# Optimization experiments

Hardware: AMD Instinct MI355X
Metric: run time of the kernel (lower is better)

## Reference

```python
import jax, jax.numpy as jnp
import numpy as np

# Dimensions (see shape_source)
U, B, D, H = 1024, 8, 512, 8
CHUNK = 32
NC = U // CHUNK          # 32 chunks
R, S, M = 32, 32, 32     # right-context rows, summary, memory
K = 31                   # depthwise conv kernel
Q = R + U + S            # 1088
KV = M + R + U           # 1088
NEG_INF = -1.0e8


def _build_attention_mask():
    """Chunk-wise Emformer mask: True = disallowed connection.
    Q layout: [R right-context rows | U utterance rows | S summary rows].
    KV layout: [M memory cols | R right-context cols | U utterance cols].
    Chunk c attends: memory banks < c, its own right-context col,
    its own chunk plus 1 left-context chunk of utterance."""
    mask = np.ones((Q, KV), dtype=bool)
    for c in range(NC):
        cols = np.zeros(KV, dtype=bool)
        cols[:min(c, M)] = True                    # memory of prior chunks
        cols[M + c] = True                         # this chunk's right context
        lo = max(0, c - 1) * CHUNK                 # 1 chunk of left context
        hi = (c + 1) * CHUNK
        cols[M + R + lo:M + R + hi] = True
        rows = [c] + list(range(R + c * CHUNK, R + (c + 1) * CHUNK)) + [R + U + c]
        mask[np.ix_(rows, np.nonzero(cols)[0])] = False
    return mask


def setup_inputs() -> dict:
    key = jax.random.key(0)
    ks = jax.random.split(key, 16)
    s = D ** -0.5
    inp = {
        'utterance': jax.random.normal(ks[0], (U, B, D), jnp.float32),
        'right_context': jax.random.normal(ks[1], (R, B, D), jnp.float32),
        'summary': jax.random.normal(ks[2], (S, B, D), jnp.float32),
        'memory': jax.random.normal(ks[3], (M, B, D), jnp.float32),
        'w_q': jax.random.normal(ks[4], (D, D), jnp.float32) * s,
        'b_q': jnp.zeros((D,), jnp.float32),
        'w_kv': jax.random.normal(ks[5], (2 * D, D), jnp.float32) * s,
        'b_kv': jnp.zeros((2 * D,), jnp.float32),
        'w_out': jax.random.normal(ks[6], (D, D), jnp.float32) * s,
        'b_out': jnp.zeros((D,), jnp.float32),
        'w_pw1': jax.random.normal(ks[7], (2 * D, D), jnp.float32) * s,
        'b_pw1': jnp.zeros((2 * D,), jnp.float32),
        'w_dw': jax.random.normal(ks[8], (D, 1, K), jnp.float32) * (K ** -0.5),
        'b_dw': jnp.zeros((D,), jnp.float32),
        'ln_g': jnp.ones((D,), jnp.float32),
        'ln_b': jnp.zeros((D,), jnp.float32),
        'w_pw2': jax.random.normal(ks[9], (D, D), jnp.float32) * s,
        'b_pw2': jnp.zeros((D,), jnp.float32),
        'lengths': jax.random.randint(ks[10], (B,), U // 2, U + 1, jnp.int32),
        'attention_mask': jnp.asarray(_build_attention_mask()),
    }
    return inp


def _conv_module(x, w_pw1, b_pw1, w_dw, b_dw, ln_g, ln_b, w_pw2, b_pw2):
    # x: (T, B, C) -> (B, C, T)
    x = x.transpose(1, 2, 0)
    x = jnp.einsum('bct,oc->bot', x, w_pw1) + b_pw1[:, None]
    a, g = jnp.split(x, 2, axis=1)
    x = a * jax.nn.sigmoid(g)                       # GLU over channel dim
    pad = (K - 1) // 2
    x = jax.lax.conv_general_dilated(
        x, w_dw, (1,), [(pad, pad)],
        dimension_numbers=('NCH', 'OIH', 'NCH'),
        feature_group_count=x.shape[1]) + b_dw[:, None]
    x = x.transpose(0, 2, 1)                        # (B, T, C) for LayerNorm
    mu = x.mean(-1, keepdims=True)
    var = ((x - mu) ** 2).mean(-1, keepdims=True)
    x = (x - mu) * jax.lax.rsqrt(var + 1e-5) * ln_g + ln_b
    x = x.transpose(0, 2, 1)
    x = x * jax.nn.sigmoid(x)                       # Swish
    x = jnp.einsum('bct,oc->bot', x, w_pw2) + b_pw2[:, None]
    return x.transpose(2, 0, 1)                     # (T, B, C)


def _emformer_forward(utterance, right_context, summary, memory,
                      w_q, b_q, w_kv, b_kv, w_out, b_out,
                      w_pw1, b_pw1, w_dw, b_dw, ln_g, ln_b, w_pw2, b_pw2,
                      lengths, attention_mask):
    d = D // H
    scaling = d ** -0.5
    q_in = jnp.concatenate([right_context, utterance, summary], axis=0)   # (Q,B,D)
    query = q_in @ w_q.T + b_q
    kv_in = jnp.concatenate([memory, right_context, utterance], axis=0)   # (KV,B,D)
    kv = kv_in @ w_kv.T + b_kv
    key_t, value_t = jnp.split(kv, 2, axis=2)

    def heads(t):  # (T,B,D) -> (B*H, T, d)
        return t.reshape(t.shape[0], B * H, d).transpose(1, 0, 2)

    qh, kh, vh = heads(query) * scaling, heads(key_t), heads(value_t)
    w = jnp.einsum('bqd,bkd->bqk', qh, kh)                                # (B*H,Q,KV)
    w = jnp.where(attention_mask[None], NEG_INF, w)
    # padding mask: pad positions are kv index >= KV - U + length
    pad = jnp.arange(KV)[None, :] >= (KV - U + lengths)[:, None]          # (B,KV)
    w = jnp.where(pad[:, None, :].repeat(H, axis=1).reshape(B * H, 1, KV), NEG_INF, w)
    p = jax.nn.softmax(w, axis=-1)
    attn = jnp.einsum('bqk,bkd->bqd', p, vh)                              # (B*H,Q,d)
    attn = attn.transpose(1, 0, 2).reshape(Q, B, D)
    outputs = attn @ w_out.T + b_out
    out_ru = outputs[:R + U]                                              # (R+U,B,D)
    # conformer convolution module with residual
    conv_out = _conv_module(out_ru, w_pw1, b_pw1, w_dw, b_dw,
                            ln_g, ln_b, w_pw2, b_pw2)
    return out_ru + conv_out


def reference(utterance, right_context, summary, memory,
              w_q, b_q, w_kv, b_kv, w_out, b_out,
              w_pw1, b_pw1, w_dw, b_dw, ln_g, ln_b, w_pw2, b_pw2,
              lengths, attention_mask):
    return _emformer_forward(utterance, right_context, summary, memory,
                             w_q, b_q, w_kv, b_kv, w_out, b_out,
                             w_pw1, b_pw1, w_dw, b_dw, ln_g, ln_b,
                             w_pw2, b_pw2, lengths, attention_mask)
```

## Files before the change

### kernel.cpp

```cpp
#include <hip/hip_runtime.h>
#include <hip/hip_bf16.h>
#include <math.h>

#define TQ    1056
#define TKV   1088

typedef __attribute__((ext_vector_type(8))) short short8;
typedef __attribute__((ext_vector_type(4))) short short4v;
typedef __attribute__((ext_vector_type(4))) float float4v;
typedef unsigned short ushort_t;

__device__ inline ushort_t f2bf(float x){
  union{float f; unsigned u;} v; v.f = x;
  unsigned r = v.u + 0x7fff + ((v.u >> 16) & 1);
  return (ushort_t)(r >> 16);
}
__device__ inline float bf2f(ushort_t h){
  union{unsigned u; float f;} v; v.u = ((unsigned)h) << 16;
  return v.f;
}

__device__ inline void gl_lds16(const ushort_t* g, ushort_t* l){
  __builtin_amdgcn_global_load_lds(
      (const __attribute__((address_space(1))) unsigned int*)g,
      (__attribute__((address_space(3))) unsigned int*)l, 16, 0, 0);
}

struct Cvt9 {
  const float* s[8];
  ushort_t*    d[8];
  const float* wdw;
  float*       wdwT;
  int bstart[9];
};

__global__ __launch_bounds__(256)
void cvt_f32_bf16(Cvt9 a)
{
  int blk = blockIdx.x;
  if (blk >= a.bstart[8]){
    int k = blk - a.bstart[8];
    int c = threadIdx.x;
    a.wdwT[k * 512 + c]       = a.wdw[c * 31 + k];
    a.wdwT[k * 512 + c + 256] = a.wdw[(c + 256) * 31 + k];
    return;
  }
  int seg = 0;
  while (blk >= a.bstart[seg + 1]) ++seg;
  int local = blk - a.bstart[seg];
  int idx = (local * 256 + threadIdx.x) * 4;
  float4v v = *(const float4v*)(a.s[seg] + idx);
  short4v o;
  #pragma unroll
  for (int j = 0; j < 4; ++j) ((ushort_t*)&o)[j] = f2bf(v[j]);
  *(short4v*)(a.d[seg] + idx) = o;
}

template<int MODE, int NX, int NT>
__global__ __launch_bounds__(256)
void gemm_bf16(const ushort_t* __restrict__ A, const ushort_t* __restrict__ Wb,
               const float* __restrict__ bias, const float* __restrict__ bias2,
               const ushort_t* __restrict__ residb,
               float* __restrict__ C0, ushort_t* __restrict__ U0,
               ushort_t* __restrict__ U1, int ny)
{
  constexpr int JN = NT / 32;
  const int blk = blockIdx.x;
  const int xcd = blk & 7;
  const int j   = blk >> 3;
  const int n_idx = j % NX;
  const int m_idx = (j / NX) * 8 + xcd;
  if (m_idx >= ny) return;

  __shared__ __align__(16) ushort_t As[128 * 64];
  __shared__ __align__(16) ushort_t Bs[NT * 64];
  const int tid  = threadIdx.x;
  const int w    = tid >> 6;
  const int lane = tid & 63;
  const int quad = lane >> 4;
  const int l16  = lane & 15;
  const int n0 = n_idx * NT;
  const int m0 = m_idx * 128;
  const int wm = (w >> 1) * 64;
  const int wn = (w & 1) * (NT / 2);
  const int srow = tid >> 3;
  const int skseg = tid & 7;

  float4v acc[4][JN];
  #pragma unroll
  for (int i = 0; i < 4; ++i)
    #pragma unroll
    for (int jj = 0; jj < JN; ++jj)
      acc[i][jj] = (float4v)(0.f);

  for (int kt = 0; kt < 8; ++kt){
    const int k0 = kt * 64;
    #pragma unroll
    for (int s = 0; s < 4; ++s){
      int row = s*32 + srow;
      gl_lds16(A + (size_t)(m0 + row) * 512 + k0 + ((skseg ^ (row & 7)) << 3),
               &As[row * 64 + (skseg << 3)]);
    }
    #pragma unroll
    for (int s = 0; s < NT/32; ++s){
      int row = s*32 + srow;
      gl_lds16(Wb + (size_t)(n0 + row) * 512 + k0 + ((skseg ^ (row & 7)) << 3),
               &Bs[row * 64 + (skseg << 3)]);
    }
    __syncthreads();
    #pragma unroll
    for (int kc = 0; kc < 2; ++kc){
      const int col = (((quad + (kc << 2)) ^ (l16 & 7)) << 3);
      short8 af[4], bf[JN];
      #pragma unroll
      for (int i = 0; i < 4; ++i)
        af[i] = *(const short8*)&As[(wm + i*16 + l16) * 64 + col];
      #pragma unroll
      for (int jj = 0; jj < JN; ++jj)
        bf[jj] = *(const short8*)&Bs[(wn + jj*16 + l16) * 64 + col];
      #pragma unroll
      for (int i = 0; i < 4; ++i)
        #pragma unroll
        for (int jj = 0; jj < JN; ++jj)
          acc[i][jj] = __builtin_amdgcn_mfma_f32_16x16x32_bf16(
                          af[i], bf[jj], acc[i][jj], 0, 0, 0);
    }
    __syncthreads();
  }

  #pragma unroll
  for (int jj = 0; jj < JN; ++jj){
    const int n = n0 + wn + jj*16 + l16;
    const float bn = (MODE == 4) ? (n < 512 ? bias[n] : bias2[n - 512])
                                 : bias[n];
    #pragma unroll
    for (int i = 0; i < 4; ++i){
      #pragma unroll
      for (int reg = 0; reg < 4; ++reg){
        const int m = m0 + wm + i*16 + quad*4 + reg;
        float v = acc[i][jj][reg] + bn;
        if (MODE == 4){
          if (n < 512){
            if (m >= 256){
              int mq = m - 256;
              int t = mq >> 3, b = mq & 7;
              int h = n >> 6, dh = n & 63;
              U0[(((size_t)(b*8 + h)) * TQ + t) * 64 + dh] = f2bf(v * 0.125f);
            }
          } else if (n < 1024){
            int n2 = n - 512;
            int t = m >> 3, b = m & 7;
            int h = n2 >> 6, dh = n2 & 63;
            U1[(((size_t)(b*8 + h)) * TKV + t) * 64 + dh] = f2bf(v);
          } else {
            int n2 = n - 1024;
            int t = m >> 3, b = m & 7;
            int h = n2 >> 6, dh = n2 & 63;
            ((ushort_t*)residb)[(((size_t)(b*8 + h)) * 64 + dh) * TKV + t] = f2bf(v);
          }
        } else if (MODE == 0){
          U0[(size_t)m * 512 + n] = f2bf(v);
        } else {
          v += bf2f(residb[(size_t)m * 512 + n]);
          C0[(size_t)m * 512 + n] = v;
        }
      }
    }
  }
}

__global__ __launch_bounds__(256)
void gemm_pw1_glu(const ushort_t* __restrict__ A, const ushort_t* __restrict__ Wb,
                  const float* __restrict__ bias, ushort_t* __restrict__ G, int ny)
{
  const int blk = blockIdx.x;
  const int xcd = blk & 7;
  const int j   = blk >> 3;
  const int n_idx = j % 8;
  const int m_idx = (j / 8) * 8 + xcd;
  if (m_idx >= ny) return;

  __shared__ __align__(16) ushort_t As [128 * 64];
  __shared__ __align__(16) ushort_t Bsa[64 * 64];
  __shared__ __align__(16) ushort_t Bsg[64 * 64];
  const int tid  = threadIdx.x;
  const int w    = tid >> 6;
  const int lane = tid & 63;
  const int quad = lane >> 4;
  const int l16  = lane & 15;
  const int n0 = n_idx * 64;
  const int m0 = m_idx * 128;
  const int wm = (w >> 1) * 64;
  const int wn = (w & 1) * 32;
  const int srow = tid >> 3;
  const int skseg = tid & 7;

  float4v acca[4][2], accg[4][2];
  #pragma unroll
  for (int i = 0; i < 4; ++i)
    #pragma unroll
    for (int jj = 0; jj < 2; ++jj){
      acca[i][jj] = (float4v)(0.f);
      accg[i][jj] = (float4v)(0.f);
    }

  for (int kt = 0; kt < 8; ++kt){
    const int k0 = kt * 64;
    #pragma unroll
    for (int s = 0; s < 4; ++s){
      int row = s*32 + srow;
      gl_lds16(A + (size_t)(m0 + row) * 512 + k0 + ((skseg ^ (row & 7)) << 3),
               &As[row * 64 + (skseg << 3)]);
    }
    #pragma unroll
    for (int s = 0; s < 2; ++s){
      int row = s*32 + srow;
      gl_lds16(Wb + (size_t)(n0 + row) * 512 + k0 + ((skseg ^ (row & 7)) << 3),
               &Bsa[row * 64 + (skseg << 3)]);
      gl_lds16(Wb + (size_t)(n0 + 512 + row) * 512 + k0 + ((skseg ^ (row & 7)) << 3),
               &Bsg[row * 64 + (skseg << 3)]);
    }
    __syncthreads();
    #pragma unroll
    for (int kc = 0; kc < 2; ++kc){
      const int col = (((quad + (kc << 2)) ^ (l16 & 7)) << 3);
      short8 af[4], ba[2], bg[2];
      #pragma unroll
      for (int i = 0; i < 4; ++i)
        af[i] = *(const short8*)&As[(wm + i*16 + l16) * 64 + col];
      #pragma unroll
      for (int jj = 0; jj < 2; ++jj){
        ba[jj] = *(const short8*)&Bsa[(wn + jj*16 + l16) * 64 + col];
        bg[jj] = *(const short8*)&Bsg[(wn + jj*16 + l16) * 64 + col];
      }
      #pragma unroll
      for (int i = 0; i < 4; ++i)
        #pragma unroll
        for (int jj = 0; jj < 2; ++jj){
          acca[i][jj] = __builtin_amdgcn_mfma_f32_16x16x32_bf16(
                           af[i], ba[jj], acca[i][jj], 0, 0, 0);
          accg[i][jj] = __builtin_amdgcn_mfma_f32_16x16x32_bf16(
                           af[i], bg[jj], accg[i][jj], 0, 0, 0);
        }
    }
    __syncthreads();
  }

  #pragma unroll
  for (int jj = 0; jj < 2; ++jj){
    const int n = n0 + wn + jj*16 + l16;
    const float bna = bias[n];
    const float bng = bias[n + 512];
    #pragma unroll
    for (int i = 0; i < 4; ++i){
      #pragma unroll
      for (int reg = 0; reg < 4; ++reg){
        const int m = m0 + wm + i*16 + quad*4 + reg;
        float a = acca[i][jj][reg] + bna;
        float g = accg[i][jj][reg] + bng;
        G[(size_t)m * 512 + n] = f2bf(a * (1.f / (1.f + __expf(-g))));
      }
    }
  }
}

#define NPAD 72
#define VPAD 136

__global__ __launch_bounds__(256)
void attn_mfma(const ushort_t* __restrict__ qh, const ushort_t* __restrict__ kh,
               const ushort_t* __restrict__ vt, const int* __restrict__ lengths,
               ushort_t* __restrict__ attn_out)
{
  const int bh = blockIdx.x;
  const int c  = blockIdx.y;
  const int b  = bh >> 3, h = bh & 7;
  const int tid = threadIdx.x;
  const int w   = tid >> 6;
  const int lane = tid & 63;
  const int quad = lane >> 4;
  const int l16  = lane & 15;
  const int len  = lengths[b];

  __shared__ __align__(16) ushort_t Qs[48 * NPAD];
  __shared__ __align__(16) ushort_t KP[128 * NPAD];
  __shared__ __align__(16) ushort_t Vt[64 * VPAD];

  const int tb2 = 64 + (c > 0 ? c - 1 : 0) * 32;
  const int tb3 = 64 + c * 32;

  for (int e = tid; e < 384; e += 256){
    int row = e >> 3, sg = (e & 7) * 8;
    short8 v = {0,0,0,0,0,0,0,0};
    if (row == 0)
      v = *(const short8*)&qh[(((size_t)bh) * TQ + c) * 64 + sg];
    else if (row >= 16)
      v = *(const short8*)&qh[(((size_t)bh) * TQ + 32 + c*32 + (row-16)) * 64 + sg];
    *(short8*)&Qs[row * NPAD + sg] = v;
  }
  for (int e = tid; e < 1024; e += 256){
    int row = e >> 3, sg = (e & 7) * 8;
    int slot = row >> 5, jj = row & 31;
    int t = (slot == 0) ? jj : (slot == 1) ? 32 + jj : (slot == 2) ? tb2 + jj : tb3 + jj;
    *(short8*)&KP[row * NPAD + sg] =
        *(const short8*)&kh[(((size_t)bh) * TKV + t) * 64 + sg];
  }
  for (int e = tid; e < 1024; e += 256){
    int dh = e >> 4, sc = (e & 15) * 8;
    int slot = sc >> 5, jj = sc & 31;
    int t = (slot == 0) ? jj : (slot == 1) ? 32 + jj : (slot == 2) ? tb2 + jj : tb3 + jj;
    *(short8*)&Vt[dh * VPAD + sc] =
        *(const short8*)&vt[(((size_t)bh) * 64 + dh) * TKV + t];
  }
  __syncthreads();

  float4v Sf[3][2];
  #pragma unroll
  for (int mt = 0; mt < 3; ++mt)
    #pragma unroll
    for (int jt = 0; jt < 2; ++jt)
      Sf[mt][jt] = (float4v)(0.f);
  #pragma unroll
  for (int kc = 0; kc < 2; ++kc){
    short8 bfr[2];
    #pragma unroll
    for (int jt = 0; jt < 2; ++jt)
      bfr[jt] = *(const short8*)&KP[(w*32 + jt*16 + l16) * NPAD + kc*32 + quad*8];
    #pragma unroll
    for (int mt = 0; mt < 3; ++mt){
      short8 afr = *(const short8*)&Qs[(mt*16 + l16) * NPAD + kc*32 + quad*8];
      #pragma unroll
      for (int jt = 0; jt < 2; ++jt)
        Sf[mt][jt] = __builtin_amdgcn_mfma_f32_16x16x32_bf16(afr, bfr[jt], Sf[mt][jt], 0,0,0);
    }
  }

  bool live[2];
  #pragma unroll
  for (int jt = 0; jt < 2; ++jt){
    int jcol = jt*16 + l16;
    if      (w == 0) live[jt] = (jcol < c);
    else if (w == 1) live[jt] = (jcol == c);
    else if (w == 2) live[jt] = (c > 0) && ((c-1)*32 + jcol < len);
    else             live[jt] = (c*32 + jcol < len);
  }
  ushort_t pb[3][2][4];
  #pragma unroll
  for (int mt = 0; mt < 3; ++mt)
    #pragma unroll
    for (int jt = 0; jt < 2; ++jt)
      #pragma unroll
      for (int r = 0; r < 4; ++r)
        pb[mt][jt][r] = live[jt] ? f2bf(__expf(Sf[mt][jt][r])) : (ushort_t)0;

  __syncthreads();

  #pragma unroll
  for (int mt = 0; mt < 3; ++mt)
    #pragma unroll
    for (int r = 0; r < 4; ++r){
      int row = mt*16 + quad*4 + r;
      KP[row * VPAD + w*32 + l16]      = pb[mt][0][r];
      KP[row * VPAD + w*32 + 16 + l16] = pb[mt][1][r];
    }
  __syncthreads();

  const short8 ones = {0x3F80,0x3F80,0x3F80,0x3F80,0x3F80,0x3F80,0x3F80,0x3F80};
  float4v Of[3], Ls[3];
  #pragma unroll
  for (int mt = 0; mt < 3; ++mt){ Of[mt] = (float4v)(0.f); Ls[mt] = (float4v)(0.f); }
  #pragma unroll
  for (int kc = 0; kc < 4; ++kc){
    short8 bv = *(const short8*)&Vt[(w*16 + l16) * VPAD + kc*32 + quad*8];
    #pragma unroll
    for (int mt = 0; mt < 3; ++mt){
      short8 ap = *(const short8*)&KP[(mt*16 + l16) * VPAD + kc*32 + quad*8];
      Of[mt] = __builtin_amdgcn_mfma_f32_16x16x32_bf16(ap, bv,   Of[mt], 0,0,0);
      Ls[mt] = __builtin_amdgcn_mfma_f32_16x16x32_bf16(ap, ones, Ls[mt], 0,0,0);
    }
  }

  #pragma unroll
  for (int mt = 0; mt < 3; ++mt){
    #pragma unroll
    for (int r = 0; r < 4; ++r){
      int row = mt*16 + quad*4 + r;
      if (mt == 0 && row != 0) continue;
      float o = Of[mt][r] / Ls[mt][r];
      int t = (mt == 0) ? c : 32 + c*32 + (row - 16);
      attn_out[(((size_t)t) * 8 + b) * 512 + h*64 + w*16 + l16] = f2bf(o);
    }
  }
}

__global__ __launch_bounds__(512)
void conv_ln_silu3(const ushort_t* __restrict__ glub,
                   const float* __restrict__ w_dwT, const float* __restrict__ b_dw,
                   const float* __restrict__ ln_g, const float* __restrict__ ln_b,
                   ushort_t* __restrict__ zb)
{
  const int b  = blockIdx.y;
  const int t0 = blockIdx.x * 16;
  const int tid = threadIdx.x;
  __shared__ __align__(16) char smem[47104];
  ushort_t* in_t = (ushort_t*)smem;
  float*    S    = (float*)smem;

  for (int e = tid; e < 2944; e += 512){
    int row = e >> 6, sg = (e & 63) * 8;
    int tt = t0 - 15 + row;
    short8 v = {0,0,0,0,0,0,0,0};
    if (tt >= 0 && tt < TQ)
      v = *(const short8*)&glub[((size_t)tt * 8 + b) * 512 + sg];
    *(short8*)&in_t[row * 512 + sg] = v;
  }
  float wreg[31];
  #pragma unroll
  for (int k = 0; k < 31; ++k) wreg[k] = w_dwT[k * 512 + tid];
  const float bd = b_dw[tid];
  __syncthreads();

  float col[46];
  #pragma unroll 2
  for (int rr = 0; rr < 46; ++rr) col[rr] = bf2f(in_t[rr * 512 + tid]);

  float r[16];
  #pragma unroll
  for (int t = 0; t < 16; ++t){
    float acc = bd;
    #pragma unroll
    for (int k = 0; k < 31; ++k) acc += col[t + k] * wreg[k];
    r[t] = acc;
  }
  __syncthreads();
  #pragma unroll
  for (int t = 0; t < 16; ++t) S[t * 512 + tid] = r[t];
  __syncthreads();

  const int tg = tid >> 5;
  const int l  = tid & 31;
  float s = 0.f;
  #pragma unroll
  for (int i = 0; i < 16; ++i) s += S[tg * 512 + l + 32*i];
  #pragma unroll
  for (int off = 16; off >= 1; off >>= 1) s += __shfl_xor(s, off);
  const float mu = s * (1.f / 512.f);
  float s2 = 0.f;
  #pragma unroll
  for (int i = 0; i < 16; ++i){
    float d = S[tg * 512 + l + 32*i] - mu;
    s2 += d * d;
  }
  #pragma unroll
  for (int off = 16; off >= 1; off >>= 1) s2 += __shfl_xor(s2, off);
  const float rs = rsqrtf(s2 * (1.f / 512.f) + 1e-5f);

  const int c0 = l * 16;
  ushort_t ov[16];
  #pragma unroll
  for (int e = 0; e < 4; ++e){
    float4v xv = *(const float4v*)&S[tg * 512 + c0 + e*4];
    float4v gv = *(const float4v*)&ln_g[c0 + e*4];
    float4v bv = *(const float4v*)&ln_b[c0 + e*4];
    #pragma unroll
    for (int jj = 0; jj < 4; ++jj){
      float xn = (xv[jj] - mu) * rs * gv[jj] + bv[jj];
      ov[e*4 + jj] = f2bf(xn * (1.f / (1.f + __expf(-xn))));
    }
  }
  const size_t obase = ((size_t)(t0 + tg) * 8 + b) * 512 + c0;
  *(short8*)&zb[obase]     = *(short8*)&ov[0];
  *(short8*)&zb[obase + 8] = *(short8*)&ov[8];
}

extern "C" void kernel_launch(void* const* d_in, const int* in_sizes, int n_in,
                              void* d_out, int out_size, void* d_ws, size_t ws_size,
                              hipStream_t stream)
{
  (void)in_sizes; (void)n_in; (void)out_size; (void)ws_size;
  const float* utter = (const float*)d_in[0];
  const float* rctx  = (const float*)d_in[1];
  const float* memry = (const float*)d_in[3];
  const float* b_q   = (const float*)d_in[5];
  const float* b_kv  = (const float*)d_in[7];
  const float* b_out = (const float*)d_in[9];
  const float* b_pw1 = (const float*)d_in[11];
  const float* w_dw  = (const float*)d_in[12];
  const float* b_dw  = (const float*)d_in[13];
  const float* ln_g  = (const float*)d_in[14];
  const float* ln_b  = (const float*)d_in[15];
  const float* b_pw2 = (const float*)d_in[17];
  const int* lengths = (const int*)d_in[18];

  ushort_t* u = (ushort_t*)d_ws;
  ushort_t* memB  = u;
  ushort_t* rcB   = memB  + 131072;
  ushort_t* uttB  = rcB   + 131072;
  ushort_t* wqB   = uttB  + 4194304;
  ushort_t* wkvB  = wqB   + 262144;
  ushort_t* woutB = wkvB  + 524288;
  ushort_t* wpw1B = woutB + 262144;
  ushort_t* wpw2B = wpw1B + 524288;
  ushort_t* q_h   = wpw2B + 262144;
  ushort_t* k_h   = q_h   + 4325376;
  ushort_t* v_t   = k_h   + 4456448;
  ushort_t* attnb = v_t   + 4456448;
  ushort_t* outru_bf = attnb + 4325376;
  float*    wdwT  = (float*)(outru_bf + 4325376);
  ushort_t* glub  = q_h;
  ushort_t* zb    = attnb;
  float* outp = (float*)d_out;

  const ushort_t* A_kv = memB;

  Cvt9 ca;
  ca.s[0] = memry;                 ca.d[0] = memB;
  ca.s[1] = rctx;                  ca.d[1] = rcB;
  ca.s[2] = utter;                 ca.d[2] = uttB;
  ca.s[3] = (const float*)d_in[4]; ca.d[3] = wqB;
  ca.s[4] = (const float*)d_in[6]; ca.d[4] = wkvB;
  ca.s[5] = (const float*)d_in[8]; ca.d[5] = woutB;
  ca.s[6] = (const float*)d_in[10];ca.d[6] = wpw1B;
  ca.s[7] = (const float*)d_in[16];ca.d[7] = wpw2B;
  ca.wdw = w_dw; ca.wdwT = wdwT;
  int cnt[8] = {131072,131072,4194304,262144,524288,262144,524288,262144};
  int acc = 0;
  for (int i = 0; i < 8; ++i){ ca.bstart[i] = acc; acc += cnt[i] / 1024; }
  ca.bstart[8] = acc;
  cvt_f32_bf16<<<dim3(acc + 31), 256, 0, stream>>>(ca);

  gemm_bf16<4, 12, 128><<<dim3(8 * 9 * 12), 256, 0, stream>>>(
      A_kv, wqB, b_q, b_kv, (const ushort_t*)v_t, nullptr, q_h, k_h, 68);
  attn_mfma<<<dim3(64, 32), 256, 0, stream>>>(q_h, k_h, v_t, lengths, attnb);
  gemm_bf16<0, 8, 64><<<dim3(8 * 9 * 8), 256, 0, stream>>>(
      attnb, woutB, b_out, nullptr, nullptr, nullptr, outru_bf, nullptr, 66);
  gemm_pw1_glu<<<dim3(8 * 9 * 8), 256, 0, stream>>>(outru_bf, wpw1B, b_pw1, glub, 66);
  conv_ln_silu3<<<dim3(66, 8), 512, 0, stream>>>(glub, wdwT, b_dw, ln_g, ln_b, zb);
  gemm_bf16<3, 8, 64><<<dim3(8 * 9 * 8), 256, 0, stream>>>(
      zb, wpw2B, b_pw2, nullptr, outru_bf, outp, nullptr, nullptr, 66);
}
```

Baseline: 257.0 us.

## Write V row-major, transpose in separate kernel, and load attention fragments directly

```diff
diff --git a/kernel.cpp b/kernel.cpp
--- a/kernel.cpp
+++ b/kernel.cpp
@@ -62,7 +62,7 @@
                const float* __restrict__ bias, const float* __restrict__ bias2,
                const ushort_t* __restrict__ residb,
                float* __restrict__ C0, ushort_t* __restrict__ U0,
-               ushort_t* __restrict__ U1, int ny)
+               ushort_t* __restrict__ U1, ushort_t* __restrict__ Uv, int ny)
 {
   constexpr int JN = NT / 32;
   const int blk = blockIdx.x;
@@ -131,7 +131,7 @@
   #pragma unroll
   for (int jj = 0; jj < JN; ++jj){
     const int n = n0 + wn + jj*16 + l16;
-    const float bn = (MODE == 4) ? (n < 512 ? bias[n] : bias2[n - 512])
+    const float bn = (MODE == 4) ? (n < 512 ? bias[n] : bias2[(n - 512) & 1023])
                                  : bias[n];
     #pragma unroll
     for (int i = 0; i < 4; ++i){
@@ -140,23 +140,19 @@
         const int m = m0 + wm + i*16 + quad*4 + reg;
         float v = acc[i][jj][reg] + bn;
         if (MODE == 4){
+          int t = m >> 3, b = m & 7;
           if (n < 512){
             if (m >= 256){
               int mq = m - 256;
-              int t = mq >> 3, b = mq & 7;
+              int tq = mq >> 3, bq = mq & 7;
               int h = n >> 6, dh = n & 63;
-              U0[(((size_t)(b*8 + h)) * TQ + t) * 64 + dh] = f2bf(v * 0.125f);
+              U0[(((size_t)(bq*8 + h)) * TQ + tq) * 64 + dh] = f2bf(v * 0.125f);
             }
-          } else if (n < 1024){
-            int n2 = n - 512;
-            int t = m >> 3, b = m & 7;
+          } else {
+            int n2 = n & 511;
             int h = n2 >> 6, dh = n2 & 63;
-            U1[(((size_t)(b*8 + h)) * TKV + t) * 64 + dh] = f2bf(v);
-          } else {
-            int n2 = n - 1024;
-            int t = m >> 3, b = m & 7;
-            int h = n2 >> 6, dh = n2 & 63;
-            ((ushort_t*)residb)[(((size_t)(b*8 + h)) * 64 + dh) * TKV + t] = f2bf(v);
+            ushort_t* dst = (n < 1024) ? U1 : Uv;
+            dst[(((size_t)(b*8 + h)) * TKV + t) * 64 + dh] = f2bf(v);
           }
         } else if (MODE == 0){
           U0[(size_t)m * 512 + n] = f2bf(v);
@@ -165,6 +161,140 @@
           C0[(size_t)m * 512 + n] = v;
         }
       }
+    }
+  }
+}
+
+__global__ __launch_bounds__(256)
+void transpose_v(const ushort_t* __restrict__ vh, ushort_t* __restrict__ vt)
+{
+  const int t0 = blockIdx.x * 64;
+  const int bh = blockIdx.y;
+  const int tid = threadIdx.x;
+  __shared__ __align__(16) ushort_t T[64 * 72];
+
+  #pragma unroll
+  for (int e = 0; e < 2; ++e){
+    int idx = e * 256 + tid;
+    int r = idx >> 3, sg = (idx & 7) * 8;
+    *(short8*)&T[r * 72 + sg] =
+        *(const short8*)&vh[(((size_t)bh) * TKV + t0 + r) * 64 + sg];
+  }
+  __syncthreads();
+
+  const int dh = tid & 63;
+  const int ts = (tid >> 6) * 16;
+  short8 v0, v1;
+  #pragma unroll
+  for (int j = 0; j < 8; ++j){
+    ((ushort_t*)&v0)[j] = T[(ts + j) * 72 + dh];
+    ((ushort_t*)&v1)[j] = T[(ts + 8 + j) * 72 + dh];
+  }
+  const size_t ob = (((size_t)bh) * 64 + dh) * TKV + t0 + ts;
+  *(short8*)&vt[ob]     = v0;
+  *(short8*)&vt[ob + 8] = v1;
+}
+
+#define PSTR 136
+
+__global__ __launch_bounds__(256)
+void attn_mfma(const ushort_t* __restrict__ qh, const ushort_t* __restrict__ kh,
+               const ushort_t* __restrict__ vt, const int* __restrict__ lengths,
+               ushort_t* __restrict__ attn_out)
+{
+  const int c  = blockIdx.x;
+  const int bh = blockIdx.y;
+  const int b  = bh >> 3, h = bh & 7;
+  const int tid = threadIdx.x;
+  const int w   = tid >> 6;
+  const int lane = tid & 63;
+  const int quad = lane >> 4;
+  const int l16  = lane & 15;
+  const int len  = lengths[b];
+  const int tb2 = 64 + (c > 0 ? c - 1 : 0) * 32;
+  const int tb3 = 64 + c * 32;
+
+  __shared__ __align__(16) ushort_t Ps[48 * PSTR];
+
+  const int basew = (w == 0) ? 0 : (w == 1) ? 32 : (w == 2) ? tb2 : tb3;
+
+  float4v Sf[3][2];
+  #pragma unroll
+  for (int mt = 0; mt < 3; ++mt)
+    #pragma unroll
+    for (int jt = 0; jt < 2; ++jt)
+      Sf[mt][jt] = (float4v)(0.f);
+
+  #pragma unroll
+  for (int kc = 0; kc < 2; ++kc){
+    short8 bfr[2];
+    #pragma unroll
+    for (int jt = 0; jt < 2; ++jt)
+      bfr[jt] = *(const short8*)&kh[((size_t)bh * TKV + basew + jt*16 + l16) * 64
+                                    + kc*32 + quad*8];
+    #pragma unroll
+    for (int mt = 0; mt < 3; ++mt){
+      int trow = (mt == 0) ? c : 32 + c*32 + (mt-1)*16 + l16;
+      short8 afr = *(const short8*)&qh[((size_t)bh * TQ + trow) * 64
+                                       + kc*32 + quad*8];
+      if (mt == 0 && l16 != 0){
+        short8 z = {0,0,0,0,0,0,0,0};
+        afr = z;
+      }
+      #pragma unroll
+      for (int jt = 0; jt < 2; ++jt)
+        Sf[mt][jt] = __builtin_amdgcn_mfma_f32_16x16x32_bf16(
+                        afr, bfr[jt], Sf[mt][jt], 0, 0, 0);
+    }
+  }
+
+  bool live[2];
+  #pragma unroll
+  for (int jt = 0; jt < 2; ++jt){
+    int jcol = jt*16 + l16;
+    if      (w == 0) live[jt] = (jcol < c);
+    else if (w == 1) live[jt] = (jcol == c);
+    else if (w == 2) live[jt] = (c > 0) && ((c-1)*32 + jcol < len);
+    else             live[jt] = (c*32 + jcol < len);
+  }
+  #pragma unroll
+  for (int mt = 0; mt < 3; ++mt)
+    #pragma unroll
+    for (int jt = 0; jt < 2; ++jt)
+      #pragma unroll
+      for (int r = 0; r < 4; ++r){
+        int row = mt*16 + quad*4 + r;
+        Ps[row * PSTR + w*32 + jt*16 + l16] =
+            live[jt] ? f2bf(__expf(Sf[mt][jt][r])) : (ushort_t)0;
+      }
+  __syncthreads();
+
+  const short8 ones = {0x3F80,0x3F80,0x3F80,0x3F80,0x3F80,0x3F80,0x3F80,0x3F80};
+  float4v Of[3], Ls[3];
+  #pragma unroll
+  for (int mt = 0; mt < 3; ++mt){ Of[mt] = (float4v)(0.f); Ls[mt] = (float4v)(0.f); }
+  #pragma unroll
+  for (int kc = 0; kc < 4; ++kc){
+    const int tbase = (kc == 0) ? 0 : (kc == 1) ? 32 : (kc == 2) ? tb2 : tb3;
+    short8 bv = *(const short8*)&vt[((size_t)bh * 64 + w*16 + l16) * TKV
+                                    + tbase + quad*8];
+    #pragma unroll
+    for (int mt = 0; mt < 3; ++mt){
+      short8 ap = *(const short8*)&Ps[(mt*16 + l16) * PSTR + kc*32 + quad*8];
+      Of[mt] = __builtin_amdgcn_mfma_f32_16x16x32_bf16(ap, bv,   Of[mt], 0,0,0);
+      Ls[mt] = __builtin_amdgcn_mfma_f32_16x16x32_bf16(ap, ones, Ls[mt], 0,0,0);
+    }
+  }
+
+  #pragma unroll
+  for (int mt = 0; mt < 3; ++mt){
+    #pragma unroll
+    for (int r = 0; r < 4; ++r){
+      int row = mt*16 + quad*4 + r;
+      if (mt == 0 && row != 0) continue;
+      float o = Of[mt][r] / Ls[mt][r];
+      int t = (mt == 0) ? c : 32 + c*32 + (row - 16);
+      attn_out[(((size_t)t) * 8 + b) * 512 + h*64 + w*16 + l16] = f2bf(o);
     }
   }
 }
@@ -264,135 +394,6 @@
   }
 }
 
-#define NPAD 72
-#define VPAD 136
-
-__global__ __launch_bounds__(256)
-void attn_mfma(const ushort_t* __restrict__ qh, const ushort_t* __restrict__ kh,
-               const ushort_t* __restrict__ vt, const int* __restrict__ lengths,
-               ushort_t* __restrict__ attn_out)
-{
-  const int bh = blockIdx.x;
-  const int c  = blockIdx.y;
-  const int b  = bh >> 3, h = bh & 7;
-  const int tid = threadIdx.x;
-  const int w   = tid >> 6;
-  const int lane = tid & 63;
-  const int quad = lane >> 4;
-  const int l16  = lane & 15;
-  const int len  = lengths[b];
-
-  __shared__ __align__(16) ushort_t Qs[48 * NPAD];
-  __shared__ __align__(16) ushort_t KP[128 * NPAD];
-  __shared__ __align__(16) ushort_t Vt[64 * VPAD];
-
-  const int tb2 = 64 + (c > 0 ? c - 1 : 0) * 32;
-  const int tb3 = 64 + c * 32;
-
-  for (int e = tid; e < 384; e += 256){
-    int row = e >> 3, sg = (e & 7) * 8;
-    short8 v = {0,0,0,0,0,0,0,0};
-    if (row == 0)
-      v = *(const short8*)&qh[(((size_t)bh) * TQ + c) * 64 + sg];
-    else if (row >= 16)
-      v = *(const short8*)&qh[(((size_t)bh) * TQ + 32 + c*32 + (row-16)) * 64 + sg];
-    *(short8*)&Qs[row * NPAD + sg] = v;
-  }
-  for (int e = tid; e < 1024; e += 256){
-    int row = e >> 3, sg = (e & 7) * 8;
-    int slot = row >> 5, jj = row & 31;
-    int t = (slot == 0) ? jj : (slot == 1) ? 32 + jj : (slot == 2) ? tb2 + jj : tb3 + jj;
-    *(short8*)&KP[row * NPAD + sg] =
-        *(const short8*)&kh[(((size_t)bh) * TKV + t) * 64 + sg];
-  }
-  for (int e = tid; e < 1024; e += 256){
-    int dh = e >> 4, sc = (e & 15) * 8;
-    int slot = sc >> 5, jj = sc & 31;
-    int t = (slot == 0) ? jj : (slot == 1) ? 32 + jj : (slot == 2) ? tb2 + jj : tb3 + jj;
-    *(short8*)&Vt[dh * VPAD + sc] =
-        *(const short8*)&vt[(((size_t)bh) * 64 + dh) * TKV + t];
-  }
-  __syncthreads();
-
-  float4v Sf[3][2];
-  #pragma unroll
-  for (int mt = 0; mt < 3; ++mt)
-    #pragma unroll
-    for (int jt = 0; jt < 2; ++jt)
-      Sf[mt][jt] = (float4v)(0.f);
-  #pragma unroll
-  for (int kc = 0; kc < 2; ++kc){
-    short8 bfr[2];
-    #pragma unroll
-    for (int jt = 0; jt < 2; ++jt)
-      bfr[jt] = *(const short8*)&KP[(w*32 + jt*16 + l16) * NPAD + kc*32 + quad*8];
-    #pragma unroll
-    for (int mt = 0; mt < 3; ++mt){
-      short8 afr = *(const short8*)&Qs[(mt*16 + l16) * NPAD + kc*32 + quad*8];
-      #pragma unroll
-      for (int jt = 0; jt < 2; ++jt)
-        Sf[mt][jt] = __builtin_amdgcn_mfma_f32_16x16x32_bf16(afr, bfr[jt], Sf[mt][jt], 0,0,0);
-    }
-  }
-
-  bool live[2];
-  #pragma unroll
-  for (int jt = 0; jt < 2; ++jt){
-    int jcol = jt*16 + l16;
-    if      (w == 0) live[jt] = (jcol < c);
-    else if (w == 1) live[jt] = (jcol == c);
-    else if (w == 2) live[jt] = (c > 0) && ((c-1)*32 + jcol < len);
-    else             live[jt] = (c*32 + jcol < len);
-  }
-  ushort_t pb[3][2][4];
-  #pragma unroll
-  for (int mt = 0; mt < 3; ++mt)
-    #pragma unroll
-    for (int jt = 0; jt < 2; ++jt)
-      #pragma unroll
-      for (int r = 0; r < 4; ++r)
-        pb[mt][jt][r] = live[jt] ? f2bf(__expf(Sf[mt][jt][r])) : (ushort_t)0;
-
-  __syncthreads();
-
-  #pragma unroll
-  for (int mt = 0; mt < 3; ++mt)
-    #pragma unroll
-    for (int r = 0; r < 4; ++r){
-      int row = mt*16 + quad*4 + r;
-      KP[row * VPAD + w*32 + l16]      = pb[mt][0][r];
-      KP[row * VPAD + w*32 + 16 + l16] = pb[mt][1][r];
-    }
-  __syncthreads();
-
-  const short8 ones = {0x3F80,0x3F80,0x3F80,0x3F80,0x3F80,0x3F80,0x3F80,0x3F80};
-  float4v Of[3], Ls[3];
-  #pragma unroll
-  for (int mt = 0; mt < 3; ++mt){ Of[mt] = (float4v)(0.f); Ls[mt] = (float4v)(0.f); }
-  #pragma unroll
-  for (int kc = 0; kc < 4; ++kc){
-    short8 bv = *(const short8*)&Vt[(w*16 + l16) * VPAD + kc*32 + quad*8];
-    #pragma unroll
-    for (int mt = 0; mt < 3; ++mt){
-      short8 ap = *(const short8*)&KP[(mt*16 + l16) * VPAD + kc*32 + quad*8];
-      Of[mt] = __builtin_amdgcn_mfma_f32_16x16x32_bf16(ap, bv,   Of[mt], 0,0,0);
-      Ls[mt] = __builtin_amdgcn_mfma_f32_16x16x32_bf16(ap, ones, Ls[mt], 0,0,0);
-    }
-  }
-
-  #pragma unroll
-  for (int mt = 0; mt < 3; ++mt){
-    #pragma unroll
-    for (int r = 0; r < 4; ++r){
-      int row = mt*16 + quad*4 + r;
-      if (mt == 0 && row != 0) continue;
-      float o = Of[mt][r] / Ls[mt][r];
-      int t = (mt == 0) ? c : 32 + c*32 + (row - 16);
-      attn_out[(((size_t)t) * 8 + b) * 512 + h*64 + w*16 + l16] = f2bf(o);
-    }
-  }
-}
-
 __global__ __launch_bounds__(512)
 void conv_ln_silu3(const ushort_t* __restrict__ glub,
                    const float* __restrict__ w_dwT, const float* __restrict__ b_dw,
@@ -503,7 +504,8 @@
   ushort_t* wpw2B = wpw1B + 524288;
   ushort_t* q_h   = wpw2B + 262144;
   ushort_t* k_h   = q_h   + 4325376;
-  ushort_t* v_t   = k_h   + 4456448;
+  ushort_t* v_h   = k_h   + 4456448;
+  ushort_t* v_t   = v_h   + 4456448;
   ushort_t* attnb = v_t   + 4456448;
   ushort_t* outru_bf = attnb + 4325376;
   float*    wdwT  = (float*)(outru_bf + 4325376);
@@ -530,12 +532,13 @@
   cvt_f32_bf16<<<dim3(acc + 31), 256, 0, stream>>>(ca);
 
   gemm_bf16<4, 12, 128><<<dim3(8 * 9 * 12), 256, 0, stream>>>(
-      A_kv, wqB, b_q, b_kv, (const ushort_t*)v_t, nullptr, q_h, k_h, 68);
-  attn_mfma<<<dim3(64, 32), 256, 0, stream>>>(q_h, k_h, v_t, lengths, attnb);
+      A_kv, wqB, b_q, b_kv, nullptr, nullptr, q_h, k_h, v_h, 68);
+  transpose_v<<<dim3(17, 64), 256, 0, stream>>>(v_h, v_t);
+  attn_mfma<<<dim3(32, 64), 256, 0, stream>>>(q_h, k_h, v_t, lengths, attnb);
   gemm_bf16<0, 8, 64><<<dim3(8 * 9 * 8), 256, 0, stream>>>(
-      attnb, woutB, b_out, nullptr, nullptr, nullptr, outru_bf, nullptr, 66);
+      attnb, woutB, b_out, nullptr, nullptr, nullptr, outru_bf, nullptr, nullptr, 66);
   gemm_pw1_glu<<<dim3(8 * 9 * 8), 256, 0, stream>>>(outru_bf, wpw1B, b_pw1, glub, 66);
   conv_ln_silu3<<<dim3(66, 8), 512, 0, stream>>>(glub, wdwT, b_dw, ln_g, ln_b, zb);
   gemm_bf16<3, 8, 64><<<dim3(8 * 9 * 8), 256, 0, stream>>>(
-      zb, wpw2B, b_pw2, nullptr, outru_bf, outp, nullptr, nullptr, 66);
-}
+      zb, wpw2B, b_pw2, nullptr, outru_bf, outp, nullptr, nullptr, nullptr, 66);
+}
```

Result: no change. 254.1 us (-1.2%).
